# Performance work log

Measured on AMD Instinct MI355X. Metric: run time of the kernel, lower is better.

The kernel has to match this reference:

```python
import jax, jax.numpy as jnp
import numpy as np

B, D, P, S, E, H = 128, 32, 13, 64, 16, 4  # batch, depth, planes, squares, embed, heads
HD = E // H  # head dim = 4


def setup_inputs() -> dict:
    key = jax.random.key(0)
    ks = jax.random.split(key, 9)
    sd = 0.05
    return {
        "board_tensor": jax.random.normal(ks[0], (B, D, P, S), dtype=jnp.float32),
        # encoder: Linear(66,64) -> ReLU -> Linear(64,16)
        "w1": jax.random.normal(ks[1], (66, 64), dtype=jnp.float32) * sd,
        "b1": jnp.zeros((64,), dtype=jnp.float32),
        "w2": jax.random.normal(ks[2], (64, E), dtype=jnp.float32) * sd,
        "b2": jnp.zeros((E,), dtype=jnp.float32),
        # MultiheadAttention in_proj (3E,E) and out_proj (E,E)
        "w_qkv": jax.random.normal(ks[3], (3 * E, E), dtype=jnp.float32) * sd,
        "b_qkv": jnp.zeros((3 * E,), dtype=jnp.float32),
        "w_out": jax.random.normal(ks[4], (E, E), dtype=jnp.float32) * sd,
        "b_out": jnp.zeros((E,), dtype=jnp.float32),
    }


def _forward(board_tensor, w1, b1, w2, b2, w_qkv, b_qkv, w_out, b_out):
    b, d, p, s = board_tensor.shape
    # per-(depth,plane) features: [64 squares, piece_id, depth_id] -> 66 dims
    piece = jnp.broadcast_to(jnp.arange(p, dtype=board_tensor.dtype)[None, None, :, None], (b, d, p, 1))
    depth = jnp.broadcast_to(jnp.arange(d, dtype=board_tensor.dtype)[None, :, None, None], (b, d, p, 1))
    feats = jnp.concatenate([board_tensor, piece, depth], axis=-1)  # (B, D, P, 66)
    h = jax.nn.relu(feats @ w1 + b1)
    enc = h @ w2 + b2  # (B, D, P, E)
    # flatten (depth, plane) into sequence, self-attention
    x = enc.reshape(b, d * p, E)  # (B, L, E)
    L = d * p
    qkv = x @ w_qkv.T + b_qkv  # (B, L, 3E)
    q, k, v = jnp.split(qkv, 3, axis=-1)
    # split heads: (B, H, L, HD)
    q = q.reshape(b, L, H, HD).transpose(0, 2, 1, 3)
    k = k.reshape(b, L, H, HD).transpose(0, 2, 1, 3)
    v = v.reshape(b, L, H, HD).transpose(0, 2, 1, 3)
    scores = jnp.einsum("bhqd,bhkd->bhqk", q, k) / jnp.sqrt(jnp.asarray(HD, x.dtype))
    attn = jax.nn.softmax(scores, axis=-1)
    out = jnp.einsum("bhqk,bhkd->bhqd", attn, v)  # (B, H, L, HD)
    out = out.transpose(0, 2, 1, 3).reshape(b, L, E)
    out = out @ w_out.T + b_out
    # dropout: identity in eval mode
    return out  # (B, L, E)


def reference(board_tensor, w1, b1, w2, b2, w_qkv, b_qkv, w_out, b_out):
    return _forward(board_tensor, w1, b1, w2, b2, w_qkv, b_qkv, w_out, b_out)
```

## Files before the change

### kernel.cpp

```cpp
#include <hip/hip_runtime.h>

#define Bn 128
#define Dd 32
#define Pp 13
#define Ee 16
#define Hh 4
#define HDim 4
#define Ll 416
#define Rr (Bn*Ll)

__device__ __forceinline__ float lane_bcast(float x, int i) {
    return __uint_as_float(__builtin_amdgcn_readlane(__float_as_uint(x), i));
}

__global__ __launch_bounds__(256, 4) void enc_qkv_kernel(
    const float* __restrict__ board, const float* __restrict__ w1,
    const float* __restrict__ b1, const float* __restrict__ w2,
    const float* __restrict__ b2, const float* __restrict__ w_qkv,
    const float* __restrict__ b_qkv,
    float* __restrict__ Q, float* __restrict__ K, float* __restrict__ V)
{
    __shared__ float sh[64 * 65];
    __shared__ float se[64 * 17];

    const int tid  = threadIdx.x;
    const int w    = tid >> 6;
    const int lane = tid & 63;
    const int row0 = blockIdx.x * 64;

    {
        float wcol[66];
        #pragma unroll
        for (int i = 0; i < 66; ++i) wcol[i] = w1[i * 64 + lane];
        const float bias1 = b1[lane];

        float fv[16];
        #pragma unroll
        for (int r = 0; r < 16; ++r)
            fv[r] = board[(size_t)(row0 + w * 16 + r) * 64 + lane];

        #pragma unroll
        for (int r = 0; r < 16; r += 2) {
            const int rowA = row0 + w * 16 + r;
            const int rowB = rowA + 1;
            const int bA = rowA / Ll, lA = rowA - bA * Ll;
            const int bB = rowB / Ll, lB = rowB - bB * Ll;
            const int dA = lA / Pp, pA = lA - dA * Pp;
            const int dB = lB / Pp, pB = lB - dB * Pp;
            float accA = bias1, accB = bias1;
            #pragma unroll
            for (int i = 0; i < 64; ++i) {
                accA = fmaf(lane_bcast(fv[r],     i), wcol[i], accA);
                accB = fmaf(lane_bcast(fv[r + 1], i), wcol[i], accB);
            }
            accA = fmaf((float)pA, wcol[64], accA);
            accB = fmaf((float)pB, wcol[64], accB);
            accA = fmaf((float)dA, wcol[65], accA);
            accB = fmaf((float)dB, wcol[65], accB);
            sh[(w * 16 + r)     * 65 + lane] = fmaxf(accA, 0.f);
            sh[(w * 16 + r + 1) * 65 + lane] = fmaxf(accB, 0.f);
        }
    }
    __syncthreads();

    {
        float4 e4 = ((const float4*)b2)[w];
        const float4* w2v = (const float4*)w2;
        #pragma unroll 4
        for (int j = 0; j < 64; ++j) {
            const float hj = sh[lane * 65 + j];
            const float4 w4 = w2v[j * 4 + w];
            e4.x = fmaf(hj, w4.x, e4.x);
            e4.y = fmaf(hj, w4.y, e4.y);
            e4.z = fmaf(hj, w4.z, e4.z);
            e4.w = fmaf(hj, w4.w, e4.w);
        }
        se[lane * 17 + 4 * w + 0] = e4.x;
        se[lane * 17 + 4 * w + 1] = e4.y;
        se[lane * 17 + 4 * w + 2] = e4.z;
        se[lane * 17 + 4 * w + 3] = e4.w;
    }
    __syncthreads();

    {
        float x[16];
        #pragma unroll
        for (int e = 0; e < 16; ++e) x[e] = se[lane * 17 + e];

        const int row = row0 + lane;
        const int b   = row / Ll;
        const int l   = row - b * Ll;

        float res[12];
        #pragma unroll
        for (int jj = 0; jj < 12; ++jj) {
            const int j = 12 * w + jj;
            const float4* wr = (const float4*)(w_qkv + j * 16);
            const float4 x0 = wr[0], x1 = wr[1], x2 = wr[2], x3 = wr[3];
            float a = b_qkv[j];
            a = fmaf(x[0],  x0.x, a); a = fmaf(x[1],  x0.y, a);
            a = fmaf(x[2],  x0.z, a); a = fmaf(x[3],  x0.w, a);
            a = fmaf(x[4],  x1.x, a); a = fmaf(x[5],  x1.y, a);
            a = fmaf(x[6],  x1.z, a); a = fmaf(x[7],  x1.w, a);
            a = fmaf(x[8],  x2.x, a); a = fmaf(x[9],  x2.y, a);
            a = fmaf(x[10], x2.z, a); a = fmaf(x[11], x2.w, a);
            a = fmaf(x[12], x3.x, a); a = fmaf(x[13], x3.y, a);
            a = fmaf(x[14], x3.z, a); a = fmaf(x[15], x3.w, a);
            res[jj] = a;
        }

        const float SC = 0.72134752044f;
        #pragma unroll
        for (int m3 = 0; m3 < 3; ++m3) {
            const int m = 3 * w + m3;
            const int tensor = m >> 2;
            const int h = m & 3;
            float4 vv = make_float4(res[4*m3+0], res[4*m3+1],
                                    res[4*m3+2], res[4*m3+3]);
            if (tensor == 0) { vv.x *= SC; vv.y *= SC; vv.z *= SC; vv.w *= SC; }
            float* basep = (tensor == 0) ? Q : (tensor == 1) ? K : V;
            *(float4*)(basep + (((size_t)(b * Hh + h)) * Ll + l) * HDim) = vv;
        }
    }
}

__global__ __launch_bounds__(256, 8) void attn_kernel(
    const float* __restrict__ Q, const float* __restrict__ K,
    const float* __restrict__ V, float* __restrict__ ATT)
{
    const int bh   = blockIdx.x;
    const int half = blockIdx.y;
    const int tid  = threadIdx.x;
    if (tid >= 208) return;
    const int qi = half * 208 + tid;

    const float4* __restrict__ Kb = (const float4*)K + (size_t)bh * Ll;
    const float4* __restrict__ Vb = (const float4*)V + (size_t)bh * Ll;
    const float4 q = ((const float4*)Q + (size_t)bh * Ll)[qi];

    float s = 0.f;
    float4 o = make_float4(0.f, 0.f, 0.f, 0.f);

    for (int l0 = 0; l0 < Ll; l0 += 8) {
        float4 kk[8], vv[8];
        #pragma unroll
        for (int j = 0; j < 8; ++j) { kk[j] = Kb[l0 + j]; vv[j] = Vb[l0 + j]; }
        #pragma unroll
        for (int j = 0; j < 8; ++j) {
            float dot = q.x * kk[j].x;
            dot = fmaf(q.y, kk[j].y, dot);
            dot = fmaf(q.z, kk[j].z, dot);
            dot = fmaf(q.w, kk[j].w, dot);
            const float e = __builtin_amdgcn_exp2f(dot);
            s += e;
            o.x = fmaf(e, vv[j].x, o.x);
            o.y = fmaf(e, vv[j].y, o.y);
            o.z = fmaf(e, vv[j].z, o.z);
            o.w = fmaf(e, vv[j].w, o.w);
        }
    }

    const int b = bh >> 2;
    const int h = bh & 3;
    const float inv = 1.0f / s;
    *(float4*)(ATT + ((size_t)(b * Ll + qi)) * Ee + h * HDim) =
        make_float4(o.x * inv, o.y * inv, o.z * inv, o.w * inv);
}

__global__ __launch_bounds__(256, 8) void outproj_kernel(
    const float* __restrict__ ATT, const float* __restrict__ w_out,
    const float* __restrict__ b_out, float* __restrict__ out)
{
    __shared__ float sx[256];
    __shared__ float sw[256];

    const int tid = threadIdx.x;
    const size_t gbase = (size_t)blockIdx.x * 256;
    sx[tid] = ATT[gbase + tid];
    sw[tid] = w_out[(tid & 15) * 16 + (tid >> 4)];
    __syncthreads();

    const int rloc = tid >> 4;
    const int o = tid & 15;
    float acc = b_out[o];
    #pragma unroll
    for (int e = 0; e < 16; ++e)
        acc = fmaf(sx[rloc * 16 + e], sw[e * 16 + o], acc);
    out[gbase + tid] = acc;
}

extern "C" void kernel_launch(void* const* d_in, const int* in_sizes, int n_in,
                              void* d_out, int out_size, void* d_ws, size_t ws_size,
                              hipStream_t stream) {
    const float* board = (const float*)d_in[0];
    const float* w1    = (const float*)d_in[1];
    const float* b1    = (const float*)d_in[2];
    const float* w2    = (const float*)d_in[3];
    const float* b2    = (const float*)d_in[4];
    const float* w_qkv = (const float*)d_in[5];
    const float* b_qkv = (const float*)d_in[6];
    const float* w_out = (const float*)d_in[7];
    const float* b_out = (const float*)d_in[8];
    float* out = (float*)d_out;

    float* ws  = (float*)d_ws;
    float* Q   = ws;
    float* K   = ws + (size_t)Rr * Ee;
    float* V   = ws + (size_t)2 * Rr * Ee;
    float* ATT = ws + (size_t)3 * Rr * Ee;

    hipLaunchKernelGGL(enc_qkv_kernel, dim3(Rr / 64), dim3(256), 0, stream,
                       board, w1, b1, w2, b2, w_qkv, b_qkv, Q, K, V);
    hipLaunchKernelGGL(attn_kernel, dim3(Bn * Hh, 2), dim3(256), 0, stream,
                       Q, K, V, ATT);
    hipLaunchKernelGGL(outproj_kernel, dim3((Rr * Ee) / 256), dim3(256), 0, stream,
                       ATT, w_out, b_out, out);
}
```

Baseline: 142.9 us.

## Fuse attention with output projection and widen encoder row blocking

Attention and the output projection now run in one kernel. The four lanes holding the four heads of a query row exchange their outputs by shuffle, and each lane computes four output columns, which removes the ATT round trip through global memory and one launch. The thread mapping changes so that the four heads of a row sit in adjacent lanes of one block, and the grid becomes (B, 7) with a tail guard. Separately, the encoder first layer now accumulates 8 rows at a time instead of 2 to expose more independent FMAs, at the cost of more live registers.

```diff
diff --git a/kernel.cpp b/kernel.cpp
--- a/kernel.cpp
+++ b/kernel.cpp
@@ -40,25 +40,35 @@
             fv[r] = board[(size_t)(row0 + w * 16 + r) * 64 + lane];
 
         #pragma unroll
-        for (int r = 0; r < 16; r += 2) {
-            const int rowA = row0 + w * 16 + r;
-            const int rowB = rowA + 1;
-            const int bA = rowA / Ll, lA = rowA - bA * Ll;
-            const int bB = rowB / Ll, lB = rowB - bB * Ll;
-            const int dA = lA / Pp, pA = lA - dA * Pp;
-            const int dB = lB / Pp, pB = lB - dB * Pp;
-            float accA = bias1, accB = bias1;
+        for (int pass = 0; pass < 2; ++pass) {
+            float a0 = bias1, a1 = bias1, a2 = bias1, a3 = bias1;
+            float a4 = bias1, a5 = bias1, a6 = bias1, a7 = bias1;
+            const int rb = pass * 8;
             #pragma unroll
             for (int i = 0; i < 64; ++i) {
-                accA = fmaf(lane_bcast(fv[r],     i), wcol[i], accA);
-                accB = fmaf(lane_bcast(fv[r + 1], i), wcol[i], accB);
+                a0 = fmaf(lane_bcast(fv[rb + 0], i), wcol[i], a0);
+                a1 = fmaf(lane_bcast(fv[rb + 1], i), wcol[i], a1);
+                a2 = fmaf(lane_bcast(fv[rb + 2], i), wcol[i], a2);
+                a3 = fmaf(lane_bcast(fv[rb + 3], i), wcol[i], a3);
+                a4 = fmaf(lane_bcast(fv[rb + 4], i), wcol[i], a4);
+                a5 = fmaf(lane_bcast(fv[rb + 5], i), wcol[i], a5);
+                a6 = fmaf(lane_bcast(fv[rb + 6], i), wcol[i], a6);
+                a7 = fmaf(lane_bcast(fv[rb + 7], i), wcol[i], a7);
             }
-            accA = fmaf((float)pA, wcol[64], accA);
-            accB = fmaf((float)pB, wcol[64], accB);
-            accA = fmaf((float)dA, wcol[65], accA);
-            accB = fmaf((float)dB, wcol[65], accB);
-            sh[(w * 16 + r)     * 65 + lane] = fmaxf(accA, 0.f);
-            sh[(w * 16 + r + 1) * 65 + lane] = fmaxf(accB, 0.f);
+            float acc[8] = {a0, a1, a2, a3, a4, a5, a6, a7};
+            #pragma unroll
+            for (int j = 0; j < 8; ++j) {
+                const int r   = w * 16 + rb + j;
+                const int row = row0 + r;
+                const int b   = row / Ll;
+                const int l   = row - b * Ll;
+                const int d   = l / Pp;
+                const int p   = l - d * Pp;
+                float a = acc[j];
+                a = fmaf((float)p, wcol[64], a);
+                a = fmaf((float)d, wcol[65], a);
+                sh[r * 65 + lane] = fmaxf(a, 0.f);
+            }
         }
     }
     __syncthreads();
@@ -124,19 +134,23 @@
     }
 }
 
-__global__ __launch_bounds__(256, 8) void attn_kernel(
+__global__ __launch_bounds__(256, 4) void attn_out_kernel(
     const float* __restrict__ Q, const float* __restrict__ K,
-    const float* __restrict__ V, float* __restrict__ ATT)
+    const float* __restrict__ V, const float* __restrict__ w_out,
+    const float* __restrict__ b_out, float* __restrict__ out)
 {
-    const int bh   = blockIdx.x;
-    const int half = blockIdx.y;
-    const int tid  = threadIdx.x;
-    if (tid >= 208) return;
-    const int qi = half * 208 + tid;
-
+    const int b   = blockIdx.x;
+    const int g   = blockIdx.y;
+    const int tid = threadIdx.x;
+    const int r   = tid >> 2;
+    const int c   = tid & 3;
+    const int l   = g * 64 + r;
+    if (l >= Ll) return;
+
+    const int bh = b * Hh + c;
     const float4* __restrict__ Kb = (const float4*)K + (size_t)bh * Ll;
     const float4* __restrict__ Vb = (const float4*)V + (size_t)bh * Ll;
-    const float4 q = ((const float4*)Q + (size_t)bh * Ll)[qi];
+    const float4 q = ((const float4*)Q + (size_t)bh * Ll)[l];
 
     float s = 0.f;
     float4 o = make_float4(0.f, 0.f, 0.f, 0.f);
@@ -160,33 +174,79 @@
         }
     }
 
-    const int b = bh >> 2;
-    const int h = bh & 3;
     const float inv = 1.0f / s;
-    *(float4*)(ATT + ((size_t)(b * Ll + qi)) * Ee + h * HDim) =
-        make_float4(o.x * inv, o.y * inv, o.z * inv, o.w * inv);
-}
-
-__global__ __launch_bounds__(256, 8) void outproj_kernel(
-    const float* __restrict__ ATT, const float* __restrict__ w_out,
-    const float* __restrict__ b_out, float* __restrict__ out)
-{
-    __shared__ float sx[256];
-    __shared__ float sw[256];
-
-    const int tid = threadIdx.x;
-    const size_t gbase = (size_t)blockIdx.x * 256;
-    sx[tid] = ATT[gbase + tid];
-    sw[tid] = w_out[(tid & 15) * 16 + (tid >> 4)];
-    __syncthreads();
-
-    const int rloc = tid >> 4;
-    const int o = tid & 15;
-    float acc = b_out[o];
-    #pragma unroll
-    for (int e = 0; e < 16; ++e)
-        acc = fmaf(sx[rloc * 16 + e], sw[e * 16 + o], acc);
-    out[gbase + tid] = acc;
+    o.x *= inv; o.y *= inv; o.z *= inv; o.w *= inv;
+
+    const int base = (tid & 63) & ~3;
+    const float4 x0 = make_float4(__shfl(o.x, base + 0), __shfl(o.y, base + 0),
+                                  __shfl(o.z, base + 0), __shfl(o.w, base + 0));
+    const float4 x1 = make_float4(__shfl(o.x, base + 1), __shfl(o.y, base + 1),
+                                  __shfl(o.z, base + 1), __shfl(o.w, base + 1));
+    const float4 x2 = make_float4(__shfl(o.x, base + 2), __shfl(o.y, base + 2),
+                                  __shfl(o.z, base + 2), __shfl(o.w, base + 2));
+    const float4 x3 = make_float4(__shfl(o.x, base + 3), __shfl(o.y, base + 3),
+                                  __shfl(o.z, base + 3), __shfl(o.w, base + 3));
+
+    const float4 bo = ((const float4*)b_out)[c];
+    float4 res;
+    {
+        const float4* wr = (const float4*)(w_out + (4 * c + 0) * 16);
+        const float4 wA = wr[0], wB = wr[1], wC = wr[2], wD = wr[3];
+        float a = bo.x;
+        a = fmaf(x0.x, wA.x, a); a = fmaf(x0.y, wA.y, a);
+        a = fmaf(x0.z, wA.z, a); a = fmaf(x0.w, wA.w, a);
+        a = fmaf(x1.x, wB.x, a); a = fmaf(x1.y, wB.y, a);
+        a = fmaf(x1.z, wB.z, a); a = fmaf(x1.w, wB.w, a);
+        a = fmaf(x2.x, wC.x, a); a = fmaf(x2.y, wC.y, a);
+        a = fmaf(x2.z, wC.z, a); a = fmaf(x2.w, wC.w, a);
+        a = fmaf(x3.x, wD.x, a); a = fmaf(x3.y, wD.y, a);
+        a = fmaf(x3.z, wD.z, a); a = fmaf(x3.w, wD.w, a);
+        res.x = a;
+    }
+    {
+        const float4* wr = (const float4*)(w_out + (4 * c + 1) * 16);
+        const float4 wA = wr[0], wB = wr[1], wC = wr[2], wD = wr[3];
+        float a = bo.y;
+        a = fmaf(x0.x, wA.x, a); a = fmaf(x0.y, wA.y, a);
+        a = fmaf(x0.z, wA.z, a); a = fmaf(x0.w, wA.w, a);
+        a = fmaf(x1.x, wB.x, a); a = fmaf(x1.y, wB.y, a);
+        a = fmaf(x1.z, wB.z, a); a = fmaf(x1.w, wB.w, a);
+        a = fmaf(x2.x, wC.x, a); a = fmaf(x2.y, wC.y, a);
+        a = fmaf(x2.z, wC.z, a); a = fmaf(x2.w, wC.w, a);
+        a = fmaf(x3.x, wD.x, a); a = fmaf(x3.y, wD.y, a);
+        a = fmaf(x3.z, wD.z, a); a = fmaf(x3.w, wD.w, a);
+        res.y = a;
+    }
+    {
+        const float4* wr = (const float4*)(w_out + (4 * c + 2) * 16);
+        const float4 wA = wr[0], wB = wr[1], wC = wr[2], wD = wr[3];
+        float a = bo.z;
+        a = fmaf(x0.x, wA.x, a); a = fmaf(x0.y, wA.y, a);
+        a = fmaf(x0.z, wA.z, a); a = fmaf(x0.w, wA.w, a);
+        a = fmaf(x1.x, wB.x, a); a = fmaf(x1.y, wB.y, a);
+        a = fmaf(x1.z, wB.z, a); a = fmaf(x1.w, wB.w, a);
+        a = fmaf(x2.x, wC.x, a); a = fmaf(x2.y, wC.y, a);
+        a = fmaf(x2.z, wC.z, a); a = fmaf(x2.w, wC.w, a);
+        a = fmaf(x3.x, wD.x, a); a = fmaf(x3.y, wD.y, a);
+        a = fmaf(x3.z, wD.z, a); a = fmaf(x3.w, wD.w, a);
+        res.z = a;
+    }
+    {
+        const float4* wr = (const float4*)(w_out + (4 * c + 3) * 16);
+        const float4 wA = wr[0], wB = wr[1], wC = wr[2], wD = wr[3];
+        float a = bo.w;
+        a = fmaf(x0.x, wA.x, a); a = fmaf(x0.y, wA.y, a);
+        a = fmaf(x0.z, wA.z, a); a = fmaf(x0.w, wA.w, a);
+        a = fmaf(x1.x, wB.x, a); a = fmaf(x1.y, wB.y, a);
+        a = fmaf(x1.z, wB.z, a); a = fmaf(x1.w, wB.w, a);
+        a = fmaf(x2.x, wC.x, a); a = fmaf(x2.y, wC.y, a);
+        a = fmaf(x2.z, wC.z, a); a = fmaf(x2.w, wC.w, a);
+        a = fmaf(x3.x, wD.x, a); a = fmaf(x3.y, wD.y, a);
+        a = fmaf(x3.z, wD.z, a); a = fmaf(x3.w, wD.w, a);
+        res.w = a;
+    }
+
+    *(float4*)(out + ((size_t)(b * Ll + l)) * Ee + 4 * c) = res;
 }
 
 extern "C" void kernel_launch(void* const* d_in, const int* in_sizes, int n_in,
@@ -207,12 +267,9 @@
     float* Q   = ws;
     float* K   = ws + (size_t)Rr * Ee;
     float* V   = ws + (size_t)2 * Rr * Ee;
-    float* ATT = ws + (size_t)3 * Rr * Ee;
 
     hipLaunchKernelGGL(enc_qkv_kernel, dim3(Rr / 64), dim3(256), 0, stream,
                        board, w1, b1, w2, b2, w_qkv, b_qkv, Q, K, V);
-    hipLaunchKernelGGL(attn_kernel, dim3(Bn * Hh, 2), dim3(256), 0, stream,
-                       Q, K, V, ATT);
-    hipLaunchKernelGGL(outproj_kernel, dim3((Rr * Ee) / 256), dim3(256), 0, stream,
-                       ATT, w_out, b_out, out);
-}
+    hipLaunchKernelGGL(attn_out_kernel, dim3(Bn, 7), dim3(256), 0, stream,
+                       Q, K, V, w_out, b_out, out);
+}
```

New measurement: 424.9 us. 197% more time.

## Restructure encoder layer-1 as row-per-lane matmul and double-buffer attention K/V loads

Applied to the files above, without the earlier changes.

The first encoder layer now stages the board tile in shared memory with coalesced float4 loads. Each lane keeps its row's 64 features in registers and computes 16 hidden units per wave, using float4 weight reads that are uniform across the wave. This replaces 64 readlane broadcasts per pair of rows and the 66-register weight column held per lane. The attention loop is rewritten to prefetch the next 4-key chunk of K/V while computing the current one, and its launch bound occupancy hint drops from 8 to 4. The cost is higher register pressure (a 64-float feature array and doubled K/V buffers), which may reduce occupancy.

```diff
diff --git a/kernel.cpp b/kernel.cpp
--- a/kernel.cpp
+++ b/kernel.cpp
@@ -9,10 +9,6 @@
 #define Ll 416
 #define Rr (Bn*Ll)
 
-__device__ __forceinline__ float lane_bcast(float x, int i) {
-    return __uint_as_float(__builtin_amdgcn_readlane(__float_as_uint(x), i));
-}
-
 __global__ __launch_bounds__(256, 4) void enc_qkv_kernel(
     const float* __restrict__ board, const float* __restrict__ w1,
     const float* __restrict__ b1, const float* __restrict__ w2,
@@ -20,7 +16,7 @@
     const float* __restrict__ b_qkv,
     float* __restrict__ Q, float* __restrict__ K, float* __restrict__ V)
 {
-    __shared__ float sh[64 * 65];
+    __shared__ float sf[64 * 65];
     __shared__ float se[64 * 17];
 
     const int tid  = threadIdx.x;
@@ -29,37 +25,56 @@
     const int row0 = blockIdx.x * 64;
 
     {
-        float wcol[66];
-        #pragma unroll
-        for (int i = 0; i < 66; ++i) wcol[i] = w1[i * 64 + lane];
-        const float bias1 = b1[lane];
-
-        float fv[16];
-        #pragma unroll
-        for (int r = 0; r < 16; ++r)
-            fv[r] = board[(size_t)(row0 + w * 16 + r) * 64 + lane];
-
-        #pragma unroll
-        for (int r = 0; r < 16; r += 2) {
-            const int rowA = row0 + w * 16 + r;
-            const int rowB = rowA + 1;
-            const int bA = rowA / Ll, lA = rowA - bA * Ll;
-            const int bB = rowB / Ll, lB = rowB - bB * Ll;
-            const int dA = lA / Pp, pA = lA - dA * Pp;
-            const int dB = lB / Pp, pB = lB - dB * Pp;
-            float accA = bias1, accB = bias1;
-            #pragma unroll
-            for (int i = 0; i < 64; ++i) {
-                accA = fmaf(lane_bcast(fv[r],     i), wcol[i], accA);
-                accB = fmaf(lane_bcast(fv[r + 1], i), wcol[i], accB);
-            }
-            accA = fmaf((float)pA, wcol[64], accA);
-            accB = fmaf((float)pB, wcol[64], accB);
-            accA = fmaf((float)dA, wcol[65], accA);
-            accB = fmaf((float)dB, wcol[65], accB);
-            sh[(w * 16 + r)     * 65 + lane] = fmaxf(accA, 0.f);
-            sh[(w * 16 + r + 1) * 65 + lane] = fmaxf(accB, 0.f);
-        }
+        const float4* bsrc = (const float4*)(board + (size_t)row0 * 64);
+        #pragma unroll
+        for (int k = 0; k < 4; ++k) {
+            const int idx = tid + 256 * k;
+            const float4 v = bsrc[idx];
+            float* dst = &sf[(idx >> 4) * 65 + 4 * (idx & 15)];
+            dst[0] = v.x; dst[1] = v.y; dst[2] = v.z; dst[3] = v.w;
+        }
+    }
+    __syncthreads();
+
+    const int row = row0 + lane;
+    const int bb  = row / Ll;
+    const int ll  = row - bb * Ll;
+    const int dd  = ll / Pp;
+    const int pp  = ll - dd * Pp;
+    const float fp = (float)pp, fd = (float)dd;
+
+    float f[64];
+    #pragma unroll
+    for (int i = 0; i < 64; ++i) f[i] = sf[lane * 65 + i];
+    __syncthreads();
+
+    #pragma unroll
+    for (int q4 = 0; q4 < 4; ++q4) {
+        const int u0 = w * 16 + q4 * 4;
+        float a0 = b1[u0 + 0], a1 = b1[u0 + 1];
+        float a2 = b1[u0 + 2], a3 = b1[u0 + 3];
+        #pragma unroll
+        for (int i = 0; i < 64; ++i) {
+            const float4 wv = *(const float4*)(w1 + i * 64 + u0);
+            a0 = fmaf(f[i], wv.x, a0);
+            a1 = fmaf(f[i], wv.y, a1);
+            a2 = fmaf(f[i], wv.z, a2);
+            a3 = fmaf(f[i], wv.w, a3);
+        }
+        {
+            const float4 wv = *(const float4*)(w1 + 64 * 64 + u0);
+            a0 = fmaf(fp, wv.x, a0); a1 = fmaf(fp, wv.y, a1);
+            a2 = fmaf(fp, wv.z, a2); a3 = fmaf(fp, wv.w, a3);
+        }
+        {
+            const float4 wv = *(const float4*)(w1 + 65 * 64 + u0);
+            a0 = fmaf(fd, wv.x, a0); a1 = fmaf(fd, wv.y, a1);
+            a2 = fmaf(fd, wv.z, a2); a3 = fmaf(fd, wv.w, a3);
+        }
+        sf[lane * 65 + u0 + 0] = fmaxf(a0, 0.f);
+        sf[lane * 65 + u0 + 1] = fmaxf(a1, 0.f);
+        sf[lane * 65 + u0 + 2] = fmaxf(a2, 0.f);
+        sf[lane * 65 + u0 + 3] = fmaxf(a3, 0.f);
     }
     __syncthreads();
 
@@ -68,7 +83,7 @@
         const float4* w2v = (const float4*)w2;
         #pragma unroll 4
         for (int j = 0; j < 64; ++j) {
-            const float hj = sh[lane * 65 + j];
+            const float hj = sf[lane * 65 + j];
             const float4 w4 = w2v[j * 4 + w];
             e4.x = fmaf(hj, w4.x, e4.x);
             e4.y = fmaf(hj, w4.y, e4.y);
@@ -86,10 +101,6 @@
         float x[16];
         #pragma unroll
         for (int e = 0; e < 16; ++e) x[e] = se[lane * 17 + e];
-
-        const int row = row0 + lane;
-        const int b   = row / Ll;
-        const int l   = row - b * Ll;
 
         float res[12];
         #pragma unroll
@@ -119,12 +130,36 @@
                                     res[4*m3+2], res[4*m3+3]);
             if (tensor == 0) { vv.x *= SC; vv.y *= SC; vv.z *= SC; vv.w *= SC; }
             float* basep = (tensor == 0) ? Q : (tensor == 1) ? K : V;
-            *(float4*)(basep + (((size_t)(b * Hh + h)) * Ll + l) * HDim) = vv;
-        }
-    }
-}
-
-__global__ __launch_bounds__(256, 8) void attn_kernel(
+            *(float4*)(basep + (((size_t)(bb * Hh + h)) * Ll + ll) * HDim) = vv;
+        }
+    }
+}
+
+#define LOADCH(kd0,kd1,kd2,kd3,vd0,vd1,vd2,vd3,c)                 \
+    { const int _l0 = (c) * 4;                                    \
+      kd0 = Kb[_l0 + 0]; kd1 = Kb[_l0 + 1];                       \
+      kd2 = Kb[_l0 + 2]; kd3 = Kb[_l0 + 3];                       \
+      vd0 = Vb[_l0 + 0]; vd1 = Vb[_l0 + 1];                       \
+      vd2 = Vb[_l0 + 2]; vd3 = Vb[_l0 + 3]; }
+
+#define COMPCH(kd0,kd1,kd2,kd3,vd0,vd1,vd2,vd3)                   \
+    { const float4 _kk[4] = {kd0, kd1, kd2, kd3};                 \
+      const float4 _vv[4] = {vd0, vd1, vd2, vd3};                 \
+      _Pragma("unroll")                                           \
+      for (int _j = 0; _j < 4; ++_j) {                            \
+          float dot = q.x * _kk[_j].x;                            \
+          dot = fmaf(q.y, _kk[_j].y, dot);                        \
+          dot = fmaf(q.z, _kk[_j].z, dot);                        \
+          dot = fmaf(q.w, _kk[_j].w, dot);                        \
+          const float e = __builtin_amdgcn_exp2f(dot);            \
+          s += e;                                                 \
+          o.x = fmaf(e, _vv[_j].x, o.x);                          \
+          o.y = fmaf(e, _vv[_j].y, o.y);                          \
+          o.z = fmaf(e, _vv[_j].z, o.z);                          \
+          o.w = fmaf(e, _vv[_j].w, o.w);                          \
+      } }
+
+__global__ __launch_bounds__(256, 4) void attn_kernel(
     const float* __restrict__ Q, const float* __restrict__ K,
     const float* __restrict__ V, float* __restrict__ ATT)
 {
@@ -141,23 +176,16 @@
     float s = 0.f;
     float4 o = make_float4(0.f, 0.f, 0.f, 0.f);
 
-    for (int l0 = 0; l0 < Ll; l0 += 8) {
-        float4 kk[8], vv[8];
-        #pragma unroll
-        for (int j = 0; j < 8; ++j) { kk[j] = Kb[l0 + j]; vv[j] = Vb[l0 + j]; }
-        #pragma unroll
-        for (int j = 0; j < 8; ++j) {
-            float dot = q.x * kk[j].x;
-            dot = fmaf(q.y, kk[j].y, dot);
-            dot = fmaf(q.z, kk[j].z, dot);
-            dot = fmaf(q.w, kk[j].w, dot);
-            const float e = __builtin_amdgcn_exp2f(dot);
-            s += e;
-            o.x = fmaf(e, vv[j].x, o.x);
-            o.y = fmaf(e, vv[j].y, o.y);
-            o.z = fmaf(e, vv[j].z, o.z);
-            o.w = fmaf(e, vv[j].w, o.w);
-        }
+    float4 kA0,kA1,kA2,kA3, vA0,vA1,vA2,vA3;
+    float4 kB0,kB1,kB2,kB3, vB0,vB1,vB2,vB3;
+
+    LOADCH(kA0,kA1,kA2,kA3,vA0,vA1,vA2,vA3, 0);
+    for (int c = 0; c < 104; c += 2) {
+        LOADCH(kB0,kB1,kB2,kB3,vB0,vB1,vB2,vB3, c + 1);
+        COMPCH(kA0,kA1,kA2,kA3,vA0,vA1,vA2,vA3);
+        if (c + 2 < 104)
+            LOADCH(kA0,kA1,kA2,kA3,vA0,vA1,vA2,vA3, c + 2);
+        COMPCH(kB0,kB1,kB2,kB3,vB0,vB1,vB2,vB3);
     }
 
     const int b = bh >> 2;
```

Result: slower. 193.1 us (+35.2%).
